# Kernel optimization log

Measured on AMD Instinct MI355X. Metric: run time of the kernel, lower is better.

Reference implementation:

```python
import jax, jax.numpy as jnp
import numpy as np

EPS = 1e-05


def _rms_norm(x, w):
    xf = x.astype(jnp.float32)
    o = xf * jax.lax.rsqrt(jnp.square(xf).mean(-1, keepdims=True) + EPS)
    return (o * w.astype(jnp.float32)).astype(x.dtype)


def _apply_rope(x, sin, cos):
    # x: [B,T,N,H]; sin/cos: [B,T,H/2]
    half = x.shape[-1] // 2
    x1, x2 = x[..., :half], x[..., half:]
    s, c = sin[:, :, None, :], cos[:, :, None, :]
    return jnp.concatenate([x1 * c - x2 * s, x2 * c + x1 * s], axis=-1).astype(x.dtype)


def setup_inputs() -> dict:
    key = jax.random.key(0)
    ks = jax.random.split(key, 12)
    B, T, D, FF, HALF = 2, 1024, 4096, 12288, 64
    return {
        "x": jax.random.normal(ks[0], (B, T, D), jnp.float32),
        "sin": jax.random.uniform(ks[1], (B, T, HALF), jnp.float32),
        "cos": jax.random.uniform(ks[2], (B, T, HALF), jnp.float32),
        "attn_norm_w": jax.random.uniform(ks[3], (D,), jnp.float32),
        "ff_norm_w": jax.random.uniform(ks[4], (D,), jnp.float32),
        "wq": jax.random.normal(ks[5], (D, D), jnp.float32) * 0.02,
        "wk": jax.random.normal(ks[6], (D, D), jnp.float32) * 0.02,
        "wv": jax.random.normal(ks[7], (D, D), jnp.float32) * 0.02,
        "wo": jax.random.normal(ks[8], (D, D), jnp.float32) * 0.02,
        "w_ff": jax.random.normal(ks[9], (D, FF), jnp.float32) * 0.02,
        "w_up": jax.random.normal(ks[10], (D, FF), jnp.float32) * 0.02,
        "w_out": jax.random.normal(ks[11], (FF, D), jnp.float32) * 0.02,
    }


def reference(x, sin, cos, attn_norm_w, ff_norm_w, wq, wk, wv, wo, w_ff, w_up, w_out):
    B, T, D = x.shape
    head_dim = sin.shape[-1] * 2  # 128
    # --- attention ---
    xn = _rms_norm(x, attn_norm_w)
    q = (xn @ wq).reshape(B, T, -1, head_dim)
    k = (xn @ wk).reshape(B, T, -1, head_dim)
    v = (xn @ wv).reshape(B, T, -1, head_dim)
    q = _apply_rope(q, sin, cos)
    k = _apply_rope(k, sin, cos)
    scale = jnp.asarray(1.0 / np.sqrt(head_dim), dtype=q.dtype)
    logits = jnp.einsum("BTNH,BSNH->BNTS", q, k) * scale
    probs = jax.nn.softmax(logits.astype(jnp.float32), axis=-1).astype(k.dtype)
    attn = jnp.einsum("BNTS,BSNH->BTNH", probs, v).reshape(B, T, D)
    x = x + attn @ wo
    # --- SwiGLU MLP ---
    res = x
    xn = _rms_norm(x, ff_norm_w)
    h = jax.nn.silu(xn @ w_ff) * (xn @ w_up)
    return res + h @ w_out
```

## Files before the change

kernel.cpp:

```cpp
#include <hip/hip_runtime.h>


#define D_MODEL 4096
#define FF_DIM  12288
#define SEQ     1024
#define NBATCH  2
#define M_ROWS  2048
#define NHEAD   32
#define HDIM    128
#define QKV_N   12288
#define FF2_N   24576

typedef short bf16x8 __attribute__((ext_vector_type(8)));
typedef ushort u16x16 __attribute__((ext_vector_type(16)));
typedef float f32x4  __attribute__((ext_vector_type(4)));

__device__ __forceinline__ ushort f2bf(float f) {
  unsigned u = __float_as_uint(f);
  u += 0x7FFFu + ((u >> 16) & 1u);
  return (ushort)(u >> 16);
}
__device__ __forceinline__ float bf2f(ushort u) {
  return __uint_as_float(((unsigned)u) << 16);
}

__device__ __forceinline__ void gload_lds16(const ushort* gsrc, ushort* ldst) {
  __builtin_amdgcn_global_load_lds((const __attribute__((address_space(1))) void*)gsrc,
                                   (__attribute__((address_space(3))) void*)ldst, 16, 0, 0);
}

#define SBAR()   asm volatile("s_barrier" ::: "memory")
#define LGKM0()  asm volatile("s_waitcnt lgkmcnt(0)" ::: "memory")
#define VMCNT8() asm volatile("s_waitcnt vmcnt(8)" ::: "memory")

__global__ __launch_bounds__(256)
void transpose_convert(const float* __restrict__ W, ushort* __restrict__ Wt,
                       int K, int N, int remap, int upoff)
{
  __shared__ float tile[64][68];
  const int t = threadIdx.x;
  const size_t k0 = (size_t)blockIdx.y * 64, n0 = (size_t)blockIdx.x * 64;
  const int lx = (t & 15) * 4, ly = t >> 4;
#pragma unroll
  for (int i = 0; i < 64; i += 16)
    *(float4*)&tile[ly + i][lx] = *(const float4*)&W[(k0 + ly + i) * N + n0 + lx];
  __syncthreads();
  const int n = t >> 2, kq = (t & 3) * 16;
  u16x16 ov;
#pragma unroll
  for (int e = 0; e < 16; e++) ov[e] = f2bf(tile[kq + e][n]);
  size_t nOut = n0 + n;
  if (remap) nOut = ((nOut >> 7) << 8) + (nOut & 127) + upoff;
  *(u16x16*)&Wt[nOut * K + k0 + kq] = ov;
}

__global__ __launch_bounds__(256)
void v_transpose(const ushort* __restrict__ v, ushort* __restrict__ vt)
{
  __shared__ ushort tile[32][33];
  const int x = threadIdx.x, y = threadIdx.y;
  const int row0 = blockIdx.x * 32;
  const int d0 = blockIdx.y * 32;
  const int h = blockIdx.z;
  const int b = row0 >> 10, sl0 = row0 & (SEQ - 1);
#pragma unroll
  for (int i = 0; i < 32; i += 8)
    tile[y + i][x] = v[(size_t)(row0 + y + i) * QKV_N + h * HDIM + d0 + x];
  __syncthreads();
  ushort* ob = vt + ((size_t)(b * NHEAD + h) * HDIM + d0) * SEQ + sl0;
#pragma unroll
  for (int i = 0; i < 32; i += 8)
    ob[(size_t)(y + i) * SEQ + x] = tile[x][y + i];
}

__global__ __launch_bounds__(256)
void rmsnorm_kernel(const float* __restrict__ x, const float* __restrict__ w,
                    ushort* __restrict__ out)
{
  const int row = blockIdx.x, t = threadIdx.x;
  const float* xr = x + (size_t)row * D_MODEL;
  float4 vv[4];
  float ss = 0.f;
#pragma unroll
  for (int p = 0; p < 4; p++) {
    vv[p] = *(const float4*)&xr[p * 1024 + t * 4];
    ss += vv[p].x * vv[p].x + vv[p].y * vv[p].y + vv[p].z * vv[p].z + vv[p].w * vv[p].w;
  }
#pragma unroll
  for (int mm = 1; mm < 64; mm <<= 1) ss += __shfl_xor(ss, mm);
  __shared__ float wsum[4];
  if ((t & 63) == 0) wsum[t >> 6] = ss;
  __syncthreads();
  ss = wsum[0] + wsum[1] + wsum[2] + wsum[3];
  const float rs = rsqrtf(ss * (1.f / 4096.f) + 1e-5f);
#pragma unroll
  for (int p = 0; p < 4; p++) {
    const float4 wv = *(const float4*)&w[p * 1024 + t * 4];
    ushort4 ov;
    ov.x = f2bf(vv[p].x * rs * wv.x);
    ov.y = f2bf(vv[p].y * rs * wv.y);
    ov.z = f2bf(vv[p].z * rs * wv.z);
    ov.w = f2bf(vv[p].w * rs * wv.w);
    *(ushort4*)&out[(size_t)row * D_MODEL + p * 1024 + t * 4] = ov;
  }
}

__global__ __launch_bounds__(256)
void rope_kernel(ushort* __restrict__ q, ushort* __restrict__ k,
                 const float* __restrict__ sinp, const float* __restrict__ cosp,
                 int ld)
{
  const size_t idx = (size_t)blockIdx.x * 256 + threadIdx.x;
  const int d = (int)(idx & 63);
  const int h = (int)((idx >> 6) & 31);
  const int t = (int)(idx >> 11);
  const float s = sinp[t * 64 + d], c = cosp[t * 64 + d];
  const size_t base = (size_t)t * ld + h * HDIM + d;
  const float q1 = bf2f(q[base]), q2 = bf2f(q[base + 64]);
  q[base]      = f2bf(q1 * c - q2 * s);
  q[base + 64] = f2bf(q2 * c + q1 * s);
  const float k1 = bf2f(k[base]), k2 = bf2f(k[base + 64]);
  k[base]      = f2bf(k1 * c - k2 * s);
  k[base + 64] = f2bf(k2 * c + k1 * s);
}

__global__ __launch_bounds__(64)
void attn_fwd(const ushort* __restrict__ q, const ushort* __restrict__ k,
              const ushort* __restrict__ vt, ushort* __restrict__ o,
              int ldq, int ldo)
{
  const int l = threadIdx.x, c16 = l & 15, g = l >> 4;
  const int qt = blockIdx.x, h = blockIdx.y, b = blockIdx.z;
  __shared__ __align__(16) ushort P_lds[16 * 32];

  const size_t head_off = (size_t)h * HDIM;
  const size_t rowQ = (size_t)(b * SEQ + qt * 16 + c16);
  const ushort* vtb = vt + (size_t)(b * NHEAD + h) * HDIM * SEQ;
  bf16x8 qf[4];
#pragma unroll
  for (int kc = 0; kc < 4; kc++)
    qf[kc] = *(const bf16x8*)(q + rowQ * ldq + head_off + kc * 32 + g * 8);

  f32x4 oacc[8];
#pragma unroll
  for (int i = 0; i < 8; i++) oacc[i] = (f32x4){0.f, 0.f, 0.f, 0.f};
  float mrow[4] = {-1e30f, -1e30f, -1e30f, -1e30f};
  float lrow[4] = {0.f, 0.f, 0.f, 0.f};
  const float scale = 0.08838834764831845f;
  const float L2E = 1.4426950408889634f;

  for (int s0 = 0; s0 < SEQ; s0 += 32) {
    f32x4 st[2];
#pragma unroll
    for (int t = 0; t < 2; t++) {
      f32x4 a = (f32x4){0.f, 0.f, 0.f, 0.f};
      const ushort* kb = k + (size_t)(b * SEQ + s0 + t * 16 + c16) * ldq + head_off + g * 8;
#pragma unroll
      for (int kc = 0; kc < 4; kc++) {
        bf16x8 kf = *(const bf16x8*)(kb + kc * 32);
        a = __builtin_amdgcn_mfma_f32_16x16x32_bf16(qf[kc], kf, a, 0, 0, 0);
      }
      st[t] = a;
    }
    float a4s[4], mn4[4], p0v[4], p1v[4];
#pragma unroll
    for (int r = 0; r < 4; r++) {
      const float s0v = st[0][r] * scale, s1v = st[1][r] * scale;
      float cm = fmaxf(s0v, s1v);
#pragma unroll
      for (int mm = 1; mm < 16; mm <<= 1) cm = fmaxf(cm, __shfl_xor(cm, mm));
      const float mn = fmaxf(mrow[r], cm);
      a4s[r] = exp2f((mrow[r] - mn) * L2E);
      mn4[r] = mn;
      p0v[r] = exp2f((s0v - mn) * L2E);
      p1v[r] = exp2f((s1v - mn) * L2E);
    }
    const f32x4 av = (f32x4){a4s[0], a4s[1], a4s[2], a4s[3]};
    const float aprod = a4s[0] * a4s[1] * a4s[2] * a4s[3];
    if (__any(aprod != 1.0f)) {
#pragma unroll
      for (int dbi = 0; dbi < 8; dbi++) oacc[dbi] *= av;
    }
#pragma unroll
    for (int r = 0; r < 4; r++) {
      float rsum = p0v[r] + p1v[r];
#pragma unroll
      for (int mm = 1; mm < 16; mm <<= 1) rsum += __shfl_xor(rsum, mm);
      lrow[r] = lrow[r] * a4s[r] + rsum;
      mrow[r] = mn4[r];
      P_lds[(g * 4 + r) * 32 + c16]      = f2bf(p0v[r]);
      P_lds[(g * 4 + r) * 32 + 16 + c16] = f2bf(p1v[r]);
    }
    __syncthreads();
    const bf16x8 pf = *(const bf16x8*)&P_lds[c16 * 32 + g * 8];
#pragma unroll
    for (int dbi = 0; dbi < 8; dbi++) {
      const bf16x8 vf = *(const bf16x8*)(vtb + (size_t)(dbi * 16 + c16) * SEQ + s0 + g * 8);
      oacc[dbi] = __builtin_amdgcn_mfma_f32_16x16x32_bf16(pf, vf, oacc[dbi], 0, 0, 0);
    }
    __syncthreads();
  }
  const size_t rowO = (size_t)(b * SEQ + qt * 16 + g * 4);
#pragma unroll
  for (int dbi = 0; dbi < 8; dbi++)
#pragma unroll
    for (int r = 0; r < 4; r++)
      o[(rowO + r) * ldo + head_off + dbi * 16 + c16] = f2bf(oacc[dbi][r] / lrow[r]);
}

template <int EPI>
__global__ __launch_bounds__(512, 2)
void gemm8p(const ushort* __restrict__ A, const ushort* __restrict__ Bt,
            const float* __restrict__ res, void* __restrict__ Cout,
            int M, int N, int K)
{
  __shared__ __align__(16) ushort lds[65536];
  const int tid = threadIdx.x;
  const int w = tid >> 6, l = tid & 63;
  const int c16 = l & 15, g = l >> 4;
  const int wr = w >> 2, wc = w & 3;

  const int nwg = gridDim.x;
  const int q8 = nwg >> 3, r8 = nwg & 7;
  const int xcd = blockIdx.x & 7, loc = blockIdx.x >> 3;
  const int wg = (xcd < r8 ? xcd * (q8 + 1) : r8 * (q8 + 1) + (xcd - r8) * q8) + loc;
  const size_t m0 = (size_t)(wg & 7) * 256;
  const size_t n0 = (size_t)(wg >> 3) * 256;
  const int nk = K >> 6;

  const int srow  = (w << 3) + (l >> 3);
  const int scolE = ((l & 7) ^ (l >> 3)) << 3;
  const ushort* gA = A  + (m0 + srow) * (size_t)K + scolE;
  const ushort* gB = Bt + (n0 + srow) * (size_t)K + scolE;

#define STG_A(p, h, q, tk)                                                        \
  gload_lds16(gA + (size_t)((h) * 128 + (q) * 64) * K + (size_t)(tk) * 64,        \
              lds + (p) * 16384 + (h) * 8192 + (q) * 4096 + (w << 9))
#define STG_B(p, h, q, tk)                                                        \
  gload_lds16(gB + (size_t)((h) * 128 + (q) * 64) * K + (size_t)(tk) * 64,        \
              lds + 32768 + (p) * 16384 + (h) * 8192 + (q) * 4096 + (w << 9))
#define STG_A2(p, h, tk) do { STG_A(p, h, 0, tk); STG_A(p, h, 1, tk); } while (0)
#define STG_B2(p, h, tk) do { STG_B(p, h, 0, tk); STG_B(p, h, 1, tk); } while (0)

  const int xorE = (c16 & 7) << 3;
  const int k0E = (g * 8) ^ xorE;
  const int k1E = (32 + g * 8) ^ xorE;
  const int aRow = wr * 64 + c16;
  const int bRow = wc * 32 + c16;

  auto LDA = [&](int p, int qm, int i, int ke) -> bf16x8 {
    return *(const bf16x8*)(lds + p * 16384 + (qm * 128 + aRow + i * 16) * 64 + ke);
  };
  auto LDB = [&](int p, int qn, int j, int ke) -> bf16x8 {
    return *(const bf16x8*)(lds + 32768 + p * 16384 + (qn * 128 + bRow + j * 16) * 64 + ke);
  };

  f32x4 acc[8][4];
#pragma unroll
  for (int i = 0; i < 8; i++)
#pragma unroll
    for (int j = 0; j < 4; j++) acc[i][j] = (f32x4){0.f, 0.f, 0.f, 0.f};
  bf16x8 a[4][2], b0[2][2], b1[2][2];

  STG_A2(0, 0, 0); STG_A2(0, 1, 0); STG_B2(0, 0, 0); STG_B2(0, 1, 0);
  STG_A2(1, 0, 1); STG_A2(1, 1, 1); STG_B2(1, 0, 1); STG_B2(1, 1, 1);
  VMCNT8(); SBAR();

  for (int t = 0; t < nk; ++t) {
    const int p = t & 1;
    const int tn2 = (t + 2 < nk) ? t + 2 : t + 2 - nk;

#pragma unroll
    for (int i = 0; i < 4; ++i) { a[i][0] = LDA(p, 0, i, k0E); a[i][1] = LDA(p, 0, i, k1E); }
#pragma unroll
    for (int j = 0; j < 2; ++j) { b0[j][0] = LDB(p, 0, j, k0E); b0[j][1] = LDB(p, 0, j, k1E); }
    SBAR(); LGKM0();
    __builtin_amdgcn_s_setprio(1);
#pragma unroll
    for (int i = 0; i < 4; ++i)
#pragma unroll
      for (int j = 0; j < 2; ++j)
#pragma unroll
        for (int kk = 0; kk < 2; ++kk)
          acc[i][j] = __builtin_amdgcn_mfma_f32_16x16x32_bf16(a[i][kk], b0[j][kk], acc[i][j], 0, 0, 0);
    __builtin_amdgcn_s_setprio(0);
    SBAR();

#pragma unroll
    for (int j = 0; j < 2; ++j) { b1[j][0] = LDB(p, 1, j, k0E); b1[j][1] = LDB(p, 1, j, k1E); }
    STG_A2(p, 0, tn2);
    STG_B2(p, 0, tn2);
    SBAR(); LGKM0();
    __builtin_amdgcn_s_setprio(1);
#pragma unroll
    for (int i = 0; i < 4; ++i)
#pragma unroll
      for (int j = 0; j < 2; ++j)
#pragma unroll
        for (int kk = 0; kk < 2; ++kk)
          acc[i][2 + j] = __builtin_amdgcn_mfma_f32_16x16x32_bf16(a[i][kk], b1[j][kk], acc[i][2 + j], 0, 0, 0);
    __builtin_amdgcn_s_setprio(0);
    SBAR();

#pragma unroll
    for (int i = 0; i < 4; ++i) { a[i][0] = LDA(p, 1, i, k0E); a[i][1] = LDA(p, 1, i, k1E); }
    STG_B2(p, 1, tn2);
    SBAR(); LGKM0();
    __builtin_amdgcn_s_setprio(1);
#pragma unroll
    for (int i = 0; i < 4; ++i)
#pragma unroll
      for (int j = 0; j < 2; ++j)
#pragma unroll
        for (int kk = 0; kk < 2; ++kk)
          acc[4 + i][j] = __builtin_amdgcn_mfma_f32_16x16x32_bf16(a[i][kk], b0[j][kk], acc[4 + i][j], 0, 0, 0);
    __builtin_amdgcn_s_setprio(0);
    SBAR();

    STG_A2(p, 1, tn2);
    SBAR(); LGKM0();
    __builtin_amdgcn_s_setprio(1);
#pragma unroll
    for (int i = 0; i < 4; ++i)
#pragma unroll
      for (int j = 0; j < 2; ++j)
#pragma unroll
        for (int kk = 0; kk < 2; ++kk)
          acc[4 + i][2 + j] = __builtin_amdgcn_mfma_f32_16x16x32_bf16(a[i][kk], b1[j][kk], acc[4 + i][2 + j], 0, 0, 0);
    __builtin_amdgcn_s_setprio(0);
    VMCNT8(); SBAR();
  }

#pragma unroll
  for (int qm = 0; qm < 2; qm++)
#pragma unroll
    for (int i = 0; i < 4; i++)
#pragma unroll
      for (int qn = 0; qn < 2; qn++)
#pragma unroll
        for (int j = 0; j < 2; j++)
#pragma unroll
          for (int r = 0; r < 4; r++) {
            const size_t row = m0 + qm * 128 + wr * 64 + i * 16 + g * 4 + r;
            if constexpr (EPI == 2) {
              if (qn == 1) continue;
              const float hv = acc[qm * 4 + i][j][r];
              const float uv = acc[qm * 4 + i][2 + j][r];
              const size_t col = (n0 >> 1) + wc * 32 + j * 16 + c16;
              ((ushort*)Cout)[row * (size_t)(N >> 1) + col] =
                  f2bf((hv / (1.f + __expf(-hv))) * uv);
            } else {
              const size_t col = n0 + qn * 128 + wc * 32 + j * 16 + c16;
              const size_t idx = row * N + col;
              const float v = acc[qm * 4 + i][qn * 2 + j][r];
              if constexpr (EPI == 0) ((ushort*)Cout)[idx] = f2bf(v);
              else                    ((float*)Cout)[idx] = res[idx] + v;
            }
          }
#undef STG_A
#undef STG_B
#undef STG_A2
#undef STG_B2
}

extern "C" void kernel_launch(void* const* d_in, const int* in_sizes, int n_in,
                              void* d_out, int out_size, void* d_ws, size_t ws_size,
                              hipStream_t stream)
{
  const float* x    = (const float*)d_in[0];
  const float* sinp = (const float*)d_in[1];
  const float* cosp = (const float*)d_in[2];
  const float* anw  = (const float*)d_in[3];
  const float* fnw  = (const float*)d_in[4];
  const float* wq   = (const float*)d_in[5];
  const float* wk   = (const float*)d_in[6];
  const float* wv   = (const float*)d_in[7];
  const float* wo   = (const float*)d_in[8];
  const float* wff  = (const float*)d_in[9];
  const float* wup  = (const float*)d_in[10];
  const float* wout = (const float*)d_in[11];
  float* out = (float*)d_out;

  const size_t szDD   = (size_t)D_MODEL * D_MODEL * 2;
  const size_t szDF   = (size_t)D_MODEL * FF_DIM * 2;
  const size_t szAct2 = (size_t)M_ROWS * D_MODEL * 2;
  const size_t szAct4 = (size_t)M_ROWS * D_MODEL * 4;
  const size_t szQKV  = (size_t)M_ROWS * QKV_N * 2;

  char* ws = (char*)d_ws;
  size_t off = 0;
  auto alloc = [&](size_t bytes) -> char* {
    char* p = ws + off;
    off += (bytes + 255) & ~(size_t)255;
    return p;
  };
  ushort* R1    = (ushort*)alloc(szDF);
  ushort* R2    = (ushort*)alloc(2 * szDF);
  ushort* wot   = (ushort*)alloc(szDD);
  ushort* xn    = (ushort*)alloc(szAct2);
  ushort* qkv   = (ushort*)alloc(szQKV);
  ushort* attnb = (ushort*)alloc(szAct2);
  float*  x2    = (float*)alloc(szAct4);
  ushort* vtb   = (ushort*)alloc(szAct2);
  if (off > ws_size) return;

  transpose_convert<<<dim3(D_MODEL / 64, D_MODEL / 64), 256, 0, stream>>>(wq, R1, D_MODEL, D_MODEL, 0, 0);
  transpose_convert<<<dim3(D_MODEL / 64, D_MODEL / 64), 256, 0, stream>>>(wk, R1 + (size_t)D_MODEL * D_MODEL, D_MODEL, D_MODEL, 0, 0);
  transpose_convert<<<dim3(D_MODEL / 64, D_MODEL / 64), 256, 0, stream>>>(wv, R1 + 2 * (size_t)D_MODEL * D_MODEL, D_MODEL, D_MODEL, 0, 0);
  transpose_convert<<<dim3(D_MODEL / 64, D_MODEL / 64), 256, 0, stream>>>(wo, wot, D_MODEL, D_MODEL, 0, 0);
  transpose_convert<<<dim3(FF_DIM / 64, D_MODEL / 64), 256, 0, stream>>>(wff, R2, D_MODEL, FF_DIM, 1, 0);
  transpose_convert<<<dim3(FF_DIM / 64, D_MODEL / 64), 256, 0, stream>>>(wup, R2, D_MODEL, FF_DIM, 1, 128);

  rmsnorm_kernel<<<M_ROWS, 256, 0, stream>>>(x, anw, xn);
  gemm8p<0><<<(M_ROWS / 256) * (QKV_N / 256), 512, 0, stream>>>(xn, R1, nullptr, qkv, M_ROWS, QKV_N, D_MODEL);
  transpose_convert<<<dim3(D_MODEL / 64, FF_DIM / 64), 256, 0, stream>>>(wout, R1, FF_DIM, D_MODEL, 0, 0);
  rope_kernel<<<(M_ROWS * NHEAD * 64) / 256, 256, 0, stream>>>(qkv, qkv + D_MODEL, sinp, cosp, QKV_N);
  v_transpose<<<dim3(M_ROWS / 32, HDIM / 32, NHEAD), dim3(32, 8), 0, stream>>>(qkv + 2 * D_MODEL, vtb);
  attn_fwd<<<dim3(SEQ / 16, NHEAD, NBATCH), 64, 0, stream>>>(qkv, qkv + D_MODEL, vtb, attnb, QKV_N, D_MODEL);
  gemm8p<1><<<(M_ROWS / 256) * (D_MODEL / 256), 512, 0, stream>>>(attnb, wot, x, x2, M_ROWS, D_MODEL, D_MODEL);

  rmsnorm_kernel<<<M_ROWS, 256, 0, stream>>>(x2, fnw, xn);
  gemm8p<2><<<(M_ROWS / 256) * (FF2_N / 256), 512, 0, stream>>>(xn, R2, nullptr, qkv , M_ROWS, FF2_N, D_MODEL);
  gemm8p<1><<<(M_ROWS / 256) * (D_MODEL / 256), 512, 0, stream>>>(qkv, R1, x2, out, M_ROWS, D_MODEL, FF_DIM);
}
```

Baseline: 1.513 ms.

## Split-K the two D-output GEMMs and software-pipeline LDS fragment loads

```diff
diff --git a/kernel.cpp b/kernel.cpp
--- a/kernel.cpp
+++ b/kernel.cpp
@@ -1,4 +1,5 @@
 #include <hip/hip_runtime.h>
+#include <type_traits>
 
 
 #define D_MODEL 4096
@@ -30,7 +31,6 @@
 }
 
 #define SBAR()   asm volatile("s_barrier" ::: "memory")
-#define LGKM0()  asm volatile("s_waitcnt lgkmcnt(0)" ::: "memory")
 #define VMCNT8() asm volatile("s_waitcnt vmcnt(8)" ::: "memory")
 
 __global__ __launch_bounds__(256)
@@ -208,11 +208,26 @@
       o[(rowO + r) * ldo + head_off + dbi * 16 + c16] = f2bf(oacc[dbi][r] / lrow[r]);
 }
 
-template <int EPI>
+__global__ __launch_bounds__(256)
+void add3_kernel(const float* __restrict__ a, const float* __restrict__ b,
+                 const float* __restrict__ c, float* __restrict__ d, int n4)
+{
+  for (int i = blockIdx.x * 256 + threadIdx.x; i < n4; i += gridDim.x * 256) {
+    const float4 av = ((const float4*)a)[i];
+    const float4 bv = ((const float4*)b)[i];
+    const float4 cv = ((const float4*)c)[i];
+    float4 dv;
+    dv.x = av.x + bv.x + cv.x; dv.y = av.y + bv.y + cv.y;
+    dv.z = av.z + bv.z + cv.z; dv.w = av.w + bv.w + cv.w;
+    ((float4*)d)[i] = dv;
+  }
+}
+
+template <int EPI, bool SPLITK>
 __global__ __launch_bounds__(512, 2)
 void gemm8p(const ushort* __restrict__ A, const ushort* __restrict__ Bt,
             const float* __restrict__ res, void* __restrict__ Cout,
-            int M, int N, int K)
+            int M, int N, int Ks, int ldk)
 {
   __shared__ __align__(16) ushort lds[65536];
   const int tid = threadIdx.x;
@@ -223,21 +238,23 @@
   const int nwg = gridDim.x;
   const int q8 = nwg >> 3, r8 = nwg & 7;
   const int xcd = blockIdx.x & 7, loc = blockIdx.x >> 3;
-  const int wg = (xcd < r8 ? xcd * (q8 + 1) : r8 * (q8 + 1) + (xcd - r8) * q8) + loc;
+  int wg = (xcd < r8 ? xcd * (q8 + 1) : r8 * (q8 + 1) + (xcd - r8) * q8) + loc;
+  int kslice = 0;
+  if constexpr (SPLITK) { kslice = wg >> 7; wg &= 127; }
   const size_t m0 = (size_t)(wg & 7) * 256;
   const size_t n0 = (size_t)(wg >> 3) * 256;
-  const int nk = K >> 6;
+  const int nk = Ks >> 6;
 
   const int srow  = (w << 3) + (l >> 3);
   const int scolE = ((l & 7) ^ (l >> 3)) << 3;
-  const ushort* gA = A  + (m0 + srow) * (size_t)K + scolE;
-  const ushort* gB = Bt + (n0 + srow) * (size_t)K + scolE;
+  const ushort* gA = A  + (size_t)kslice * Ks + (m0 + srow) * (size_t)ldk + scolE;
+  const ushort* gB = Bt + (size_t)kslice * Ks + (n0 + srow) * (size_t)ldk + scolE;
 
 #define STG_A(p, h, q, tk)                                                        \
-  gload_lds16(gA + (size_t)((h) * 128 + (q) * 64) * K + (size_t)(tk) * 64,        \
+  gload_lds16(gA + (size_t)((h) * 128 + (q) * 64) * ldk + (size_t)(tk) * 64,      \
               lds + (p) * 16384 + (h) * 8192 + (q) * 4096 + (w << 9))
 #define STG_B(p, h, q, tk)                                                        \
-  gload_lds16(gB + (size_t)((h) * 128 + (q) * 64) * K + (size_t)(tk) * 64,        \
+  gload_lds16(gB + (size_t)((h) * 128 + (q) * 64) * ldk + (size_t)(tk) * 64,      \
               lds + 32768 + (p) * 16384 + (h) * 8192 + (q) * 4096 + (w << 9))
 #define STG_A2(p, h, tk) do { STG_A(p, h, 0, tk); STG_A(p, h, 1, tk); } while (0)
 #define STG_B2(p, h, tk) do { STG_B(p, h, 0, tk); STG_B(p, h, 1, tk); } while (0)
@@ -260,21 +277,23 @@
   for (int i = 0; i < 8; i++)
 #pragma unroll
     for (int j = 0; j < 4; j++) acc[i][j] = (f32x4){0.f, 0.f, 0.f, 0.f};
-  bf16x8 a[4][2], b0[2][2], b1[2][2];
-
-  STG_A2(0, 0, 0); STG_A2(0, 1, 0); STG_B2(0, 0, 0); STG_B2(0, 1, 0);
-  STG_A2(1, 0, 1); STG_A2(1, 1, 1); STG_B2(1, 0, 1); STG_B2(1, 1, 1);
-  VMCNT8(); SBAR();
-
-  for (int t = 0; t < nk; ++t) {
-    const int p = t & 1;
-    const int tn2 = (t + 2 < nk) ? t + 2 : t + 2 - nk;
-
-#pragma unroll
-    for (int i = 0; i < 4; ++i) { a[i][0] = LDA(p, 0, i, k0E); a[i][1] = LDA(p, 0, i, k1E); }
-#pragma unroll
-    for (int j = 0; j < 2; ++j) { b0[j][0] = LDB(p, 0, j, k0E); b0[j][1] = LDB(p, 0, j, k1E); }
-    SBAR(); LGKM0();
+
+  bf16x8 a0[4][2], a1[4][2], b0A[2][2], b0B[2][2], b1[2][2];
+
+  STG_A2(0, 0, 0); STG_B2(0, 0, 0); STG_B2(0, 1, 0); STG_A2(0, 1, 0);
+  STG_A2(1, 0, 1); STG_B2(1, 0, 1); STG_B2(1, 1, 1); STG_A2(1, 1, 1);
+  VMCNT8();
+  SBAR();
+#pragma unroll
+  for (int j = 0; j < 2; ++j) { b0A[j][0] = LDB(0, 0, j, k0E); b0A[j][1] = LDB(0, 0, j, k1E); }
+#pragma unroll
+  for (int i = 0; i < 4; ++i) { a0[i][0] = LDA(0, 0, i, k0E); a0[i][1] = LDA(0, 0, i, k1E); }
+
+  auto tile = [&](auto Pc, auto& b0C, auto& b0N, int tn2) {
+    constexpr int P = decltype(Pc)::value;
+#pragma unroll
+    for (int j = 0; j < 2; ++j) { b1[j][0] = LDB(P, 1, j, k0E); b1[j][1] = LDB(P, 1, j, k1E); }
+    SBAR();
     __builtin_amdgcn_s_setprio(1);
 #pragma unroll
     for (int i = 0; i < 4; ++i)
@@ -282,15 +301,13 @@
       for (int j = 0; j < 2; ++j)
 #pragma unroll
         for (int kk = 0; kk < 2; ++kk)
-          acc[i][j] = __builtin_amdgcn_mfma_f32_16x16x32_bf16(a[i][kk], b0[j][kk], acc[i][j], 0, 0, 0);
+          acc[i][j] = __builtin_amdgcn_mfma_f32_16x16x32_bf16(a0[i][kk], b0C[j][kk], acc[i][j], 0, 0, 0);
     __builtin_amdgcn_s_setprio(0);
     SBAR();
-
-#pragma unroll
-    for (int j = 0; j < 2; ++j) { b1[j][0] = LDB(p, 1, j, k0E); b1[j][1] = LDB(p, 1, j, k1E); }
-    STG_A2(p, 0, tn2);
-    STG_B2(p, 0, tn2);
-    SBAR(); LGKM0();
+#pragma unroll
+    for (int i = 0; i < 4; ++i) { a1[i][0] = LDA(P, 1, i, k0E); a1[i][1] = LDA(P, 1, i, k1E); }
+    STG_A2(P, 0, tn2); STG_B2(P, 0, tn2);
+    SBAR();
     __builtin_amdgcn_s_setprio(1);
 #pragma unroll
     for (int i = 0; i < 4; ++i)
@@ -298,14 +315,14 @@
       for (int j = 0; j < 2; ++j)
 #pragma unroll
         for (int kk = 0; kk < 2; ++kk)
-          acc[i][2 + j] = __builtin_amdgcn_mfma_f32_16x16x32_bf16(a[i][kk], b1[j][kk], acc[i][2 + j], 0, 0, 0);
+          acc[i][2 + j] = __builtin_amdgcn_mfma_f32_16x16x32_bf16(a0[i][kk], b1[j][kk], acc[i][2 + j], 0, 0, 0);
     __builtin_amdgcn_s_setprio(0);
-    SBAR();
-
-#pragma unroll
-    for (int i = 0; i < 4; ++i) { a[i][0] = LDA(p, 1, i, k0E); a[i][1] = LDA(p, 1, i, k1E); }
-    STG_B2(p, 1, tn2);
-    SBAR(); LGKM0();
+    VMCNT8();
+    SBAR();
+#pragma unroll
+    for (int j = 0; j < 2; ++j) { b0N[j][0] = LDB(P ^ 1, 0, j, k0E); b0N[j][1] = LDB(P ^ 1, 0, j, k1E); }
+    STG_B2(P, 1, tn2);
+    SBAR();
     __builtin_amdgcn_s_setprio(1);
 #pragma unroll
     for (int i = 0; i < 4; ++i)
@@ -313,12 +330,13 @@
       for (int j = 0; j < 2; ++j)
 #pragma unroll
         for (int kk = 0; kk < 2; ++kk)
-          acc[4 + i][j] = __builtin_amdgcn_mfma_f32_16x16x32_bf16(a[i][kk], b0[j][kk], acc[4 + i][j], 0, 0, 0);
+          acc[4 + i][j] = __builtin_amdgcn_mfma_f32_16x16x32_bf16(a1[i][kk], b0C[j][kk], acc[4 + i][j], 0, 0, 0);
     __builtin_amdgcn_s_setprio(0);
     SBAR();
-
-    STG_A2(p, 1, tn2);
-    SBAR(); LGKM0();
+#pragma unroll
+    for (int i = 0; i < 4; ++i) { a0[i][0] = LDA(P ^ 1, 0, i, k0E); a0[i][1] = LDA(P ^ 1, 0, i, k1E); }
+    STG_A2(P, 1, tn2);
+    SBAR();
     __builtin_amdgcn_s_setprio(1);
 #pragma unroll
     for (int i = 0; i < 4; ++i)
@@ -326,9 +344,17 @@
       for (int j = 0; j < 2; ++j)
 #pragma unroll
         for (int kk = 0; kk < 2; ++kk)
-          acc[4 + i][2 + j] = __builtin_amdgcn_mfma_f32_16x16x32_bf16(a[i][kk], b1[j][kk], acc[4 + i][2 + j], 0, 0, 0);
+          acc[4 + i][2 + j] = __builtin_amdgcn_mfma_f32_16x16x32_bf16(a1[i][kk], b1[j][kk], acc[4 + i][2 + j], 0, 0, 0);
     __builtin_amdgcn_s_setprio(0);
-    VMCNT8(); SBAR();
+    VMCNT8();
+    SBAR();
+  };
+
+  for (int t = 0; t < nk; t += 2) {
+    const int tn2a = (t + 2 < nk) ? t + 2 : t + 2 - nk;
+    const int tn2b = (t + 3 < nk) ? t + 3 : t + 3 - nk;
+    tile(std::integral_constant<int, 0>{}, b0A, b0B, tn2a);
+    tile(std::integral_constant<int, 1>{}, b0B, b0A, tn2b);
   }
 
 #pragma unroll
@@ -353,8 +379,9 @@
               const size_t col = n0 + qn * 128 + wc * 32 + j * 16 + c16;
               const size_t idx = row * N + col;
               const float v = acc[qm * 4 + i][qn * 2 + j][r];
-              if constexpr (EPI == 0) ((ushort*)Cout)[idx] = f2bf(v);
-              else                    ((float*)Cout)[idx] = res[idx] + v;
+              if constexpr (EPI == 0)      ((ushort*)Cout)[idx] = f2bf(v);
+              else if constexpr (EPI == 1) ((float*)Cout)[idx] = res[idx] + v;
+              else                         ((float*)Cout)[(size_t)kslice * M * N + idx] = v;
             }
           }
 #undef STG_A
@@ -386,6 +413,7 @@
   const size_t szAct2 = (size_t)M_ROWS * D_MODEL * 2;
   const size_t szAct4 = (size_t)M_ROWS * D_MODEL * 4;
   const size_t szQKV  = (size_t)M_ROWS * QKV_N * 2;
+  const size_t MN     = (size_t)M_ROWS * D_MODEL;
 
   char* ws = (char*)d_ws;
   size_t off = 0;
@@ -402,6 +430,7 @@
   ushort* attnb = (ushort*)alloc(szAct2);
   float*  x2    = (float*)alloc(szAct4);
   ushort* vtb   = (ushort*)alloc(szAct2);
+  float*  part  = (float*)alloc(2 * MN * 4);
   if (off > ws_size) return;
 
   transpose_convert<<<dim3(D_MODEL / 64, D_MODEL / 64), 256, 0, stream>>>(wq, R1, D_MODEL, D_MODEL, 0, 0);
@@ -412,14 +441,16 @@
   transpose_convert<<<dim3(FF_DIM / 64, D_MODEL / 64), 256, 0, stream>>>(wup, R2, D_MODEL, FF_DIM, 1, 128);
 
   rmsnorm_kernel<<<M_ROWS, 256, 0, stream>>>(x, anw, xn);
-  gemm8p<0><<<(M_ROWS / 256) * (QKV_N / 256), 512, 0, stream>>>(xn, R1, nullptr, qkv, M_ROWS, QKV_N, D_MODEL);
+  gemm8p<0, false><<<(M_ROWS / 256) * (QKV_N / 256), 512, 0, stream>>>(xn, R1, nullptr, qkv, M_ROWS, QKV_N, D_MODEL, D_MODEL);
   transpose_convert<<<dim3(D_MODEL / 64, FF_DIM / 64), 256, 0, stream>>>(wout, R1, FF_DIM, D_MODEL, 0, 0);
   rope_kernel<<<(M_ROWS * NHEAD * 64) / 256, 256, 0, stream>>>(qkv, qkv + D_MODEL, sinp, cosp, QKV_N);
   v_transpose<<<dim3(M_ROWS / 32, HDIM / 32, NHEAD), dim3(32, 8), 0, stream>>>(qkv + 2 * D_MODEL, vtb);
   attn_fwd<<<dim3(SEQ / 16, NHEAD, NBATCH), 64, 0, stream>>>(qkv, qkv + D_MODEL, vtb, attnb, QKV_N, D_MODEL);
-  gemm8p<1><<<(M_ROWS / 256) * (D_MODEL / 256), 512, 0, stream>>>(attnb, wot, x, x2, M_ROWS, D_MODEL, D_MODEL);
+  gemm8p<3, true><<<256, 512, 0, stream>>>(attnb, wot, nullptr, part, M_ROWS, D_MODEL, D_MODEL / 2, D_MODEL);
+  add3_kernel<<<2048, 256, 0, stream>>>(x, part, part + MN, x2, (int)(MN / 4));
 
   rmsnorm_kernel<<<M_ROWS, 256, 0, stream>>>(x2, fnw, xn);
-  gemm8p<2><<<(M_ROWS / 256) * (FF2_N / 256), 512, 0, stream>>>(xn, R2, nullptr, qkv , M_ROWS, FF2_N, D_MODEL);
-  gemm8p<1><<<(M_ROWS / 256) * (D_MODEL / 256), 512, 0, stream>>>(qkv, R1, x2, out, M_ROWS, D_MODEL, FF_DIM);
-}
+  gemm8p<2, false><<<(M_ROWS / 256) * (FF2_N / 256), 512, 0, stream>>>(xn, R2, nullptr, qkv , M_ROWS, FF2_N, D_MODEL, D_MODEL);
+  gemm8p<3, true><<<256, 512, 0, stream>>>(qkv, R1, nullptr, part, M_ROWS, D_MODEL, FF_DIM / 2, FF_DIM);
+  add3_kernel<<<2048, 256, 0, stream>>>(x2, part, part + MN, out, (int)(MN / 4));
+}
```

Result: slower. 3.215 ms (+112.5%).

## Split-K the two D-output GEMMs into two slices and reduce with residual

Applied to the files above, without the earlier changes.

```diff
diff --git a/kernel.cpp b/kernel.cpp
--- a/kernel.cpp
+++ b/kernel.cpp
@@ -208,11 +208,26 @@
       o[(rowO + r) * ldo + head_off + dbi * 16 + c16] = f2bf(oacc[dbi][r] / lrow[r]);
 }
 
-template <int EPI>
+__global__ __launch_bounds__(256)
+void add3_kernel(const float* __restrict__ a, const float* __restrict__ b,
+                 const float* __restrict__ c, float* __restrict__ d, int n4)
+{
+  for (int i = blockIdx.x * 256 + threadIdx.x; i < n4; i += gridDim.x * 256) {
+    const float4 av = ((const float4*)a)[i];
+    const float4 bv = ((const float4*)b)[i];
+    const float4 cv = ((const float4*)c)[i];
+    float4 dv;
+    dv.x = av.x + bv.x + cv.x; dv.y = av.y + bv.y + cv.y;
+    dv.z = av.z + bv.z + cv.z; dv.w = av.w + bv.w + cv.w;
+    ((float4*)d)[i] = dv;
+  }
+}
+
+template <int EPI, bool SPLITK>
 __global__ __launch_bounds__(512, 2)
 void gemm8p(const ushort* __restrict__ A, const ushort* __restrict__ Bt,
             const float* __restrict__ res, void* __restrict__ Cout,
-            int M, int N, int K)
+            int M, int N, int Ks, int ldk)
 {
   __shared__ __align__(16) ushort lds[65536];
   const int tid = threadIdx.x;
@@ -223,21 +238,23 @@
   const int nwg = gridDim.x;
   const int q8 = nwg >> 3, r8 = nwg & 7;
   const int xcd = blockIdx.x & 7, loc = blockIdx.x >> 3;
-  const int wg = (xcd < r8 ? xcd * (q8 + 1) : r8 * (q8 + 1) + (xcd - r8) * q8) + loc;
+  int wg = (xcd < r8 ? xcd * (q8 + 1) : r8 * (q8 + 1) + (xcd - r8) * q8) + loc;
+  int kslice = 0;
+  if constexpr (SPLITK) { kslice = wg >> 7; wg &= 127; }
   const size_t m0 = (size_t)(wg & 7) * 256;
   const size_t n0 = (size_t)(wg >> 3) * 256;
-  const int nk = K >> 6;
+  const int nk = Ks >> 6;
 
   const int srow  = (w << 3) + (l >> 3);
   const int scolE = ((l & 7) ^ (l >> 3)) << 3;
-  const ushort* gA = A  + (m0 + srow) * (size_t)K + scolE;
-  const ushort* gB = Bt + (n0 + srow) * (size_t)K + scolE;
+  const ushort* gA = A  + (size_t)kslice * Ks + (m0 + srow) * (size_t)ldk + scolE;
+  const ushort* gB = Bt + (size_t)kslice * Ks + (n0 + srow) * (size_t)ldk + scolE;
 
 #define STG_A(p, h, q, tk)                                                        \
-  gload_lds16(gA + (size_t)((h) * 128 + (q) * 64) * K + (size_t)(tk) * 64,        \
+  gload_lds16(gA + (size_t)((h) * 128 + (q) * 64) * ldk + (size_t)(tk) * 64,      \
               lds + (p) * 16384 + (h) * 8192 + (q) * 4096 + (w << 9))
 #define STG_B(p, h, q, tk)                                                        \
-  gload_lds16(gB + (size_t)((h) * 128 + (q) * 64) * K + (size_t)(tk) * 64,        \
+  gload_lds16(gB + (size_t)((h) * 128 + (q) * 64) * ldk + (size_t)(tk) * 64,      \
               lds + 32768 + (p) * 16384 + (h) * 8192 + (q) * 4096 + (w << 9))
 #define STG_A2(p, h, tk) do { STG_A(p, h, 0, tk); STG_A(p, h, 1, tk); } while (0)
 #define STG_B2(p, h, tk) do { STG_B(p, h, 0, tk); STG_B(p, h, 1, tk); } while (0)
@@ -353,8 +370,9 @@
               const size_t col = n0 + qn * 128 + wc * 32 + j * 16 + c16;
               const size_t idx = row * N + col;
               const float v = acc[qm * 4 + i][qn * 2 + j][r];
-              if constexpr (EPI == 0) ((ushort*)Cout)[idx] = f2bf(v);
-              else                    ((float*)Cout)[idx] = res[idx] + v;
+              if constexpr (EPI == 0)      ((ushort*)Cout)[idx] = f2bf(v);
+              else if constexpr (EPI == 1) ((float*)Cout)[idx] = res[idx] + v;
+              else                         ((float*)Cout)[(size_t)kslice * M * N + idx] = v;
             }
           }
 #undef STG_A
@@ -386,6 +404,7 @@
   const size_t szAct2 = (size_t)M_ROWS * D_MODEL * 2;
   const size_t szAct4 = (size_t)M_ROWS * D_MODEL * 4;
   const size_t szQKV  = (size_t)M_ROWS * QKV_N * 2;
+  const size_t MN     = (size_t)M_ROWS * D_MODEL;
 
   char* ws = (char*)d_ws;
   size_t off = 0;
@@ -402,6 +421,7 @@
   ushort* attnb = (ushort*)alloc(szAct2);
   float*  x2    = (float*)alloc(szAct4);
   ushort* vtb   = (ushort*)alloc(szAct2);
+  float*  part  = (float*)alloc(2 * MN * 4);
   if (off > ws_size) return;
 
   transpose_convert<<<dim3(D_MODEL / 64, D_MODEL / 64), 256, 0, stream>>>(wq, R1, D_MODEL, D_MODEL, 0, 0);
@@ -412,14 +432,16 @@
   transpose_convert<<<dim3(FF_DIM / 64, D_MODEL / 64), 256, 0, stream>>>(wup, R2, D_MODEL, FF_DIM, 1, 128);
 
   rmsnorm_kernel<<<M_ROWS, 256, 0, stream>>>(x, anw, xn);
-  gemm8p<0><<<(M_ROWS / 256) * (QKV_N / 256), 512, 0, stream>>>(xn, R1, nullptr, qkv, M_ROWS, QKV_N, D_MODEL);
+  gemm8p<0, false><<<(M_ROWS / 256) * (QKV_N / 256), 512, 0, stream>>>(xn, R1, nullptr, qkv, M_ROWS, QKV_N, D_MODEL, D_MODEL);
   transpose_convert<<<dim3(D_MODEL / 64, FF_DIM / 64), 256, 0, stream>>>(wout, R1, FF_DIM, D_MODEL, 0, 0);
   rope_kernel<<<(M_ROWS * NHEAD * 64) / 256, 256, 0, stream>>>(qkv, qkv + D_MODEL, sinp, cosp, QKV_N);
   v_transpose<<<dim3(M_ROWS / 32, HDIM / 32, NHEAD), dim3(32, 8), 0, stream>>>(qkv + 2 * D_MODEL, vtb);
   attn_fwd<<<dim3(SEQ / 16, NHEAD, NBATCH), 64, 0, stream>>>(qkv, qkv + D_MODEL, vtb, attnb, QKV_N, D_MODEL);
-  gemm8p<1><<<(M_ROWS / 256) * (D_MODEL / 256), 512, 0, stream>>>(attnb, wot, x, x2, M_ROWS, D_MODEL, D_MODEL);
+  gemm8p<3, true><<<256, 512, 0, stream>>>(attnb, wot, nullptr, part, M_ROWS, D_MODEL, D_MODEL / 2, D_MODEL);
+  add3_kernel<<<2048, 256, 0, stream>>>(x, part, part + MN, x2, (int)(MN / 4));
 
   rmsnorm_kernel<<<M_ROWS, 256, 0, stream>>>(x2, fnw, xn);
-  gemm8p<2><<<(M_ROWS / 256) * (FF2_N / 256), 512, 0, stream>>>(xn, R2, nullptr, qkv , M_ROWS, FF2_N, D_MODEL);
-  gemm8p<1><<<(M_ROWS / 256) * (D_MODEL / 256), 512, 0, stream>>>(qkv, R1, x2, out, M_ROWS, D_MODEL, FF_DIM);
-}
+  gemm8p<2, false><<<(M_ROWS / 256) * (FF2_N / 256), 512, 0, stream>>>(xn, R2, nullptr, qkv , M_ROWS, FF2_N, D_MODEL, D_MODEL);
+  gemm8p<3, true><<<256, 512, 0, stream>>>(qkv, R1, nullptr, part, M_ROWS, D_MODEL, FF_DIM / 2, FF_DIM);
+  add3_kernel<<<2048, 256, 0, stream>>>(x2, part, part + MN, out, (int)(MN / 4));
+}
```

New measurement: 1.369 ms. 9.5% less time.
